# Kernel optimization log

Hardware: AMD Instinct MI355X
Metric: run time of the kernel (lower is better)

The kernel has to match this reference:

```python
import jax, jax.numpy as jnp
import numpy as np

B, S, D = 4, 1024, 768
H = 12
DK = D // H            # 64
NUM_EMB = 10
MAX_DIST = 100000.0 * 2 ** 0.5
POS_SCALE = 100000.0   # tile positions live in [0, 100000]


def setup_inputs() -> dict:
    key = jax.random.key(0)
    ks = jax.random.split(key, 12)
    query = jax.random.normal(ks[0], (B, S, D), dtype=jnp.float32)
    key_t = jax.random.normal(ks[1], (B, S, D), dtype=jnp.float32)
    value = jax.random.normal(ks[2], (B, S, D), dtype=jnp.float32)
    tile_positions = jax.random.uniform(ks[3], (B, S, 2), dtype=jnp.float32) * POS_SCALE
    # Linear weights, torch layout [out, in]; xavier_uniform init, zero bias
    lim = float(np.sqrt(6.0 / (D + D)))
    Wq = jax.random.uniform(ks[4], (D, D), minval=-lim, maxval=lim, dtype=jnp.float32)
    Wk = jax.random.uniform(ks[5], (D, D), minval=-lim, maxval=lim, dtype=jnp.float32)
    Wv = jax.random.uniform(ks[6], (D, D), minval=-lim, maxval=lim, dtype=jnp.float32)
    bq = jnp.zeros((D,), jnp.float32)
    bk = jnp.zeros((D,), jnp.float32)
    bv = jnp.zeros((D,), jnp.float32)
    emb_k = jax.random.normal(ks[7], (NUM_EMB, DK), dtype=jnp.float32)  # nn.Embedding default N(0,1)
    return {"query": query, "key": key_t, "value": value,
            "tile_positions": tile_positions,
            "Wq": Wq, "bq": bq, "Wk": Wk, "bk": bk, "Wv": Wv, "bv": bv,
            "emb_k": emb_k}


def reference(query, key, value, tile_positions, Wq, bq, Wk, bk, Wv, bv, emb_k):
    b, s, _ = query.shape
    # projections -> [B, H, S, DK]
    q = (query @ Wq.T + bq).reshape(b, s, H, DK).transpose(0, 2, 1, 3)
    k = (key   @ Wk.T + bk).reshape(b, s, H, DK).transpose(0, 2, 1, 3)
    v = (value @ Wv.T + bv).reshape(b, s, H, DK).transpose(0, 2, 1, 3)
    # pairwise distances, normalized, discretized to embedding indices
    pos = jax.lax.stop_gradient(tile_positions)
    diff = pos[:, :, None, :] - pos[:, None, :, :]          # [B,S,S,2]
    dist = jnp.sqrt(jnp.sum(diff * diff, axis=-1)) / MAX_DIST  # [B,S,S]
    idx = jnp.clip(jnp.round(dist * (NUM_EMB - 1)), 0, NUM_EMB - 1).astype(jnp.int32)
    rk = emb_k[idx]                                          # [B,S,S,DK]
    # logits: QK^T plus distance-aware key bias
    attn_logits = jnp.einsum('bhqd,bhkd->bhqk', q, k)
    attn_logits = attn_logits + jnp.einsum('bhqd,bqkd->bhqk', q, rk)
    attn_logits = attn_logits / (DK ** 0.5)
    attention = jax.nn.softmax(attn_logits, axis=-1)
    out = jnp.einsum('bhqk,bhkd->bhqd', attention, v)       # [B,H,S,DK]
    out = out.transpose(0, 2, 1, 3).reshape(b, s, -1)       # [B,S,D]
    return out
```

## Files before the change

kernel.cpp:

```cpp
#include <hip/hip_runtime.h>
#include <hip/hip_bf16.h>

#define Bsz 4
#define Ssz 1024
#define Dsz 768
#define Hn 12
#define DKsz 64
#define NUMEMB 10

#define IDX_OFF 64
#define K_OFF   4194368
#define V_OFF   10485824
#define WBF_OFF 16777280
#define XBF_OFF 20316224
#define WS_TIER_B 20316224ULL
#define WS_TIER_A 39190592ULL

#define NXz 3145728
#define NWz 589824

#define IPAD 80

typedef __attribute__((ext_vector_type(8))) short short8;
typedef __attribute__((ext_vector_type(8))) float float8;
typedef __attribute__((ext_vector_type(4))) float f32x4;
typedef __attribute__((ext_vector_type(4))) unsigned int u32x4;

__device__ __forceinline__ float bfbits2f(short u) {
    union { unsigned int i; float f; } v;
    v.i = ((unsigned int)(unsigned short)u) << 16;
    return v.f;
}
__device__ __forceinline__ unsigned short f2bf_bits(float f) {
    __hip_bfloat16 h = __float2bfloat16(f);
    return *reinterpret_cast<unsigned short*>(&h);
}

template<int CTRL>
__device__ __forceinline__ float dppf(float x) {
    int xi = __float_as_int(x);
    int r = __builtin_amdgcn_update_dpp(xi, xi, CTRL, 0xF, 0xF, true);
    return __int_as_float(r);
}
__device__ __forceinline__ float red_max16(float v) {
    v = fmaxf(v, dppf<0xB1>(v));
    v = fmaxf(v, dppf<0x4E>(v));
    v = fmaxf(v, dppf<0x124>(v));
    v = fmaxf(v, dppf<0x128>(v));
    return v;
}
__device__ __forceinline__ float red_sum16(float v) {
    v += dppf<0xB1>(v);
    v += dppf<0x4E>(v);
    v += dppf<0x124>(v);
    v += dppf<0x128>(v);
    return v;
}

template<bool BF16>
__device__ __forceinline__ float loadf(const void* base, size_t idx) {
    if constexpr (BF16) return __bfloat162float(((const __hip_bfloat16*)base)[idx]);
    else return ((const float*)base)[idx];
}
template<bool BF16>
__device__ __forceinline__ short8 load8bf(const void* base, size_t idx) {
    if constexpr (BF16) {
        return *(const short8*)((const short*)base + idx);
    } else {
        float8 f = *(const float8*)((const float*)base + idx);
        short8 r;
#pragma unroll
        for (int i = 0; i < 8; i++) r[i] = (short)f2bf_bits(f[i]);
        return r;
    }
}
template<bool BF16>
__device__ __forceinline__ float8 load8f(const void* base, size_t idx) {
    if constexpr (BF16) {
        short8 s = *(const short8*)((const short*)base + idx);
        float8 f;
#pragma unroll
        for (int i = 0; i < 8; i++) f[i] = bfbits2f(s[i]);
        return f;
    } else {
        return *(const float8*)((const float*)base + idx);
    }
}

__global__ __launch_bounds__(64) void detect_kernel(
    const unsigned int* __restrict__ q, const unsigned int* __restrict__ p,
    const unsigned int* __restrict__ w, const unsigned int* __restrict__ e,
    int* __restrict__ flags)
{
    const int which = blockIdx.x;
    const unsigned int* ptr = (which == 0) ? q : ((which == 1) ? p : ((which == 2) ? w : e));
    const int n = (which == 3) ? 320 : ((which == 1) ? 4096 : 1024);
    int cnt = 0;
    for (int i = threadIdx.x; i < n; i += 64) {
        const unsigned int ex = (ptr[i] >> 7) & 0xFF;
        cnt += (ex >= 110 && ex <= 145) ? 1 : 0;
    }
#pragma unroll
    for (int off = 1; off < 64; off <<= 1) cnt += __shfl_xor(cnt, off, 64);
    if (threadIdx.x == 0) flags[which] = (2 * cnt > n) ? 1 : 0;
}

__global__ __launch_bounds__(256) void conv_kernel(
    const void* __restrict__ X0, const void* __restrict__ X1, const void* __restrict__ X2,
    const void* __restrict__ W0, const void* __restrict__ W1, const void* __restrict__ W2,
    const int* __restrict__ flags, short* __restrict__ Xbf, short* __restrict__ Wbf,
    int doX)
{
    const long t = (long)blockIdx.x * 256 + threadIdx.x;
    const bool xb = flags[0] != 0, wb = flags[2] != 0;
    if (doX) {
        const long i8 = t * 8;
        if (i8 < (long)3 * NXz) {
            const int z = (int)(i8 / NXz);
            const long off = i8 - (long)z * NXz;
            const void* X = (z == 0) ? X0 : ((z == 1) ? X1 : X2);
            short8 v = xb ? load8bf<true>(X, off) : load8bf<false>(X, off);
            *(short8*)(Xbf + i8) = v;
        } else {
            const long j = i8 - (long)3 * NXz;
            const int z = (int)(j / NWz);
            const long off = j - (long)z * NWz;
            const void* W = (z == 0) ? W0 : ((z == 1) ? W1 : W2);
            short8 v = wb ? load8bf<true>(W, off) : load8bf<false>(W, off);
            *(short8*)(Wbf + j) = v;
        }
    } else {
        const long j = t * 8;
        const int z = (int)(j / NWz);
        const long off = j - (long)z * NWz;
        const void* W = (z == 0) ? W0 : ((z == 1) ? W1 : W2);
        short8 v = wb ? load8bf<true>(W, off) : load8bf<false>(W, off);
        *(short8*)(Wbf + j) = v;
    }
}

template<bool PB>
__device__ __forceinline__ void idx_body(
    const void* pos, unsigned char* __restrict__ idxb)
{
    const int kt = blockIdx.x, qt = blockIdx.y, b = blockIdx.z;
    const int t = threadIdx.x;
    const int r = t >> 2, cc = t & 3;
    const int q = qt * 64 + r;
    const float qx = loadf<PB>(pos, ((size_t)b * Ssz + q) * 2);
    const float qy = loadf<PB>(pos, ((size_t)b * Ssz + q) * 2 + 1);
    const float MAXD = 141421.35623730951f;
    const int k0 = kt * 64 + cc * 16;
    unsigned int w[4];
#pragma unroll
    for (int g = 0; g < 4; g++) {
        unsigned int acc = 0;
#pragma unroll
        for (int u = 0; u < 4; u++) {
            const int k = k0 + g * 4 + u;
            const float kx = loadf<PB>(pos, ((size_t)b * Ssz + k) * 2);
            const float ky = loadf<PB>(pos, ((size_t)b * Ssz + k) * 2 + 1);
            const float dx = __fsub_rn(qx, kx);
            const float dy = __fsub_rn(qy, ky);
            const float ss = __fadd_rn(__fmul_rn(dx, dx), __fmul_rn(dy, dy));
            const float dist = __fdiv_rn(sqrtf(ss), MAXD);
            const float d9 = __fmul_rn(dist, 9.0f);
            int idx = (int)rintf(d9);
            idx = idx < 0 ? 0 : (idx > NUMEMB - 1 ? NUMEMB - 1 : idx);
            acc |= ((unsigned int)idx) << (8 * u);
        }
        w[g] = acc;
    }
    u32x4 v; v[0] = w[0]; v[1] = w[1]; v[2] = w[2]; v[3] = w[3];
    *(u32x4*)(idxb + ((size_t)(b * Ssz + q)) * Ssz + k0) = v;
}

__global__ __launch_bounds__(256) void idx_kernel(
    const void* pos, const int* __restrict__ flags, unsigned char* __restrict__ idxb)
{
    if (flags[1] != 0) idx_body<true >(pos, idxb);
    else               idx_body<false>(pos, idxb);
}

template<bool XB, bool WB>
__device__ __forceinline__ void proj_body(
    const void* X, const void* W, const void* bias, bool biasbf, void* Y, bool ybf,
    int bx, int by, short* As, short* Bs)
{
    const int tid  = threadIdx.x;
    const int wave = tid >> 6;
    const int lane = tid & 63;
    const int l15  = lane & 15;
    const int quad = lane >> 4;
    const int wm = wave & 1;
    const int wn = wave >> 1;
    const int m0 = bx * 64;
    const int n0 = by * 128;

    f32x4 acc[2][4];
#pragma unroll
    for (int i = 0; i < 2; i++)
#pragma unroll
        for (int j = 0; j < 4; j++) acc[i][j] = (f32x4)0.0f;

    const int r0 = tid >> 3;
    const int cc = tid & 7;

    short8 pa0 = load8bf<XB>(X, (size_t)(m0 + r0)      * Dsz + cc * 8);
    short8 pa1 = load8bf<XB>(X, (size_t)(m0 + 32 + r0) * Dsz + cc * 8);
    short8 pb0 = load8bf<WB>(W, (size_t)(n0 + r0)      * Dsz + cc * 8);
    short8 pb1 = load8bf<WB>(W, (size_t)(n0 + 32 + r0) * Dsz + cc * 8);
    short8 pb2 = load8bf<WB>(W, (size_t)(n0 + 64 + r0) * Dsz + cc * 8);
    short8 pb3 = load8bf<WB>(W, (size_t)(n0 + 96 + r0) * Dsz + cc * 8);

    for (int kk = 0; kk < Dsz; kk += 64) {
        __syncthreads();
        *(short8*)&As[(r0)      * 72 + cc * 8] = pa0;
        *(short8*)&As[(32 + r0) * 72 + cc * 8] = pa1;
        *(short8*)&Bs[(r0)      * 72 + cc * 8] = pb0;
        *(short8*)&Bs[(32 + r0) * 72 + cc * 8] = pb1;
        *(short8*)&Bs[(64 + r0) * 72 + cc * 8] = pb2;
        *(short8*)&Bs[(96 + r0) * 72 + cc * 8] = pb3;
        __syncthreads();

        if (kk + 64 < Dsz) {
            const int k2 = kk + 64 + cc * 8;
            pa0 = load8bf<XB>(X, (size_t)(m0 + r0)      * Dsz + k2);
            pa1 = load8bf<XB>(X, (size_t)(m0 + 32 + r0) * Dsz + k2);
            pb0 = load8bf<WB>(W, (size_t)(n0 + r0)      * Dsz + k2);
            pb1 = load8bf<WB>(W, (size_t)(n0 + 32 + r0) * Dsz + k2);
            pb2 = load8bf<WB>(W, (size_t)(n0 + 64 + r0) * Dsz + k2);
            pb3 = load8bf<WB>(W, (size_t)(n0 + 96 + r0) * Dsz + k2);
        }

#pragma unroll
        for (int st = 0; st < 2; st++) {
            short8 af[2], bf[4];
#pragma unroll
            for (int i = 0; i < 2; i++)
                af[i] = *(const short8*)&As[(wm * 32 + i * 16 + l15) * 72 + st * 32 + quad * 8];
#pragma unroll
            for (int j = 0; j < 4; j++)
                bf[j] = *(const short8*)&Bs[(wn * 64 + j * 16 + l15) * 72 + st * 32 + quad * 8];
#pragma unroll
            for (int i = 0; i < 2; i++)
#pragma unroll
                for (int j = 0; j < 4; j++)
                    acc[i][j] = __builtin_amdgcn_mfma_f32_16x16x32_bf16(af[i], bf[j], acc[i][j], 0, 0, 0);
        }
    }

#pragma unroll
    for (int j = 0; j < 4; j++) {
        const int n = n0 + wn * 64 + j * 16 + l15;
        const float bv_ = biasbf ? loadf<true>(bias, n) : loadf<false>(bias, n);
#pragma unroll
        for (int i = 0; i < 2; i++) {
#pragma unroll
            for (int r = 0; r < 4; r++) {
                const int m = m0 + wm * 32 + i * 16 + quad * 4 + r;
                const float val = acc[i][j][r] + bv_;
                if (ybf) ((__hip_bfloat16*)Y)[(size_t)m * Dsz + n] = __float2bfloat16(val);
                else     ((float*)Y)[(size_t)m * Dsz + n] = val;
            }
        }
    }
}

__global__ __launch_bounds__(256) void proj_kernel(
    const void* X0, const void* X1, const void* X2,
    const void* Wq, const void* bq, const void* Wk, const void* bk,
    const void* Wv, const void* bv,
    void* Qw, void* Kw, void* Vw, const int* __restrict__ flags,
    int fx, int fw)
{
    __shared__ __align__(16) short As[64 * 72];
    __shared__ __align__(16) short Bs[128 * 72];
    const int z = blockIdx.z;
    const void* X = (z == 0) ? X0 : ((z == 1) ? X1 : X2);
    const void* W = (z == 0) ? Wq : ((z == 1) ? Wk : Wv);
    const void* B = (z == 0) ? bq : ((z == 1) ? bk : bv);
    void* Y = (z == 0) ? Qw : ((z == 1) ? Kw : Vw);
    const bool xb = fx || flags[0] != 0;
    const bool wb = fw || flags[2] != 0;
    const bool biasbf = flags[2] != 0;
    const bool ybf = (flags[0] != 0) || (z != 0);
    if (xb) { if (wb) proj_body<true , true >(X, W, B, biasbf, Y, ybf, blockIdx.x, blockIdx.y, As, Bs);
              else    proj_body<true , false>(X, W, B, biasbf, Y, ybf, blockIdx.x, blockIdx.y, As, Bs); }
    else    { if (wb) proj_body<false, true >(X, W, B, biasbf, Y, ybf, blockIdx.x, blockIdx.y, As, Bs);
              else    proj_body<false, false>(X, W, B, biasbf, Y, ybf, blockIdx.x, blockIdx.y, As, Bs); }
}

template<bool QB, bool EB>
__device__ __forceinline__ void attn_body(
    const void* Qw, const short* __restrict__ Ks, const short* __restrict__ Vs,
    const unsigned char* __restrict__ idxb, const void* __restrict__ emb, void* out,
    unsigned short* Klds, unsigned short* Vtlds, unsigned short* Plds,
    float* qe, unsigned char* Ilds)
{
    const int qt = blockIdx.x, h = blockIdx.y, b = blockIdx.z;
    const int tid  = threadIdx.x;
    const int wave = tid >> 6;
    const int lane = tid & 63;
    const int l15  = lane & 15;
    const int quad = lane >> 4;

    for (int p = tid; p < 64 * NUMEMB; p += 256) {
        const int row = p / NUMEMB, e = p - row * NUMEMB;
        const size_t qoff = ((size_t)b * Ssz + qt * 64 + row) * Dsz + h * DKsz;
        float s = 0.f;
#pragma unroll
        for (int c = 0; c < 8; c++) {
            short8 qv = load8bf<QB>(Qw, qoff + c * 8);
            float8 ef = load8f<EB>(emb, (size_t)e * DKsz + c * 8);
#pragma unroll
            for (int i = 0; i < 8; i++) s += bfbits2f(qv[i]) * ef[i];
        }
        qe[p] = s;
    }

    short8 qfrag[2];
    {
        const size_t qbase = ((size_t)b * Ssz + qt * 64 + wave * 16 + l15) * Dsz + h * DKsz;
        qfrag[0] = load8bf<QB>(Qw, qbase + quad * 8);
        qfrag[1] = load8bf<QB>(Qw, qbase + 32 + quad * 8);
    }

    float m_run[4], l_run[4];
    f32x4 oacc[4];
#pragma unroll
    for (int r = 0; r < 4; r++) { m_run[r] = -1e30f; l_run[r] = 0.f; }
#pragma unroll
    for (int j = 0; j < 4; j++) oacc[j] = (f32x4)0.0f;

    const int srow = tid >> 3, schk = tid & 7;
    const int vp   = tid >> 3;
    const int irow = tid >> 2, ichk = tid & 3;

    short8 pk0, pk1, pv0, pv1;
    u32x4 pidx;
    {
        pk0 = *(const short8*)(Ks + ((size_t)b * Ssz + srow)       * Dsz + h * DKsz + schk * 8);
        pk1 = *(const short8*)(Ks + ((size_t)b * Ssz + 32 + srow)  * Dsz + h * DKsz + schk * 8);
        pv0 = *(const short8*)(Vs + ((size_t)b * Ssz + 2 * vp)     * Dsz + h * DKsz + schk * 8);
        pv1 = *(const short8*)(Vs + ((size_t)b * Ssz + 2 * vp + 1) * Dsz + h * DKsz + schk * 8);
        pidx = *(const u32x4*)(idxb + ((size_t)(b * Ssz + irow)) * Ssz + qt * 64 + ichk * 16);
    }

    for (int it = 0; it < 16; it++) {
        __syncthreads();
        *(short8*)&Klds[(srow)      * 72 + schk * 8] = pk0;
        *(short8*)&Klds[(32 + srow) * 72 + schk * 8] = pk1;
        {
            const int ssw = (2 * vp) ^ (schk << 3);
#pragma unroll
            for (int i = 0; i < 8; i++) {
                const unsigned int dw = (unsigned int)(unsigned short)pv0[i]
                                      | ((unsigned int)(unsigned short)pv1[i] << 16);
                *(unsigned int*)&Vtlds[(schk * 8 + i) * 72 + ssw] = dw;
            }
        }
        *(u32x4*)&Ilds[irow * IPAD + ichk * 16] = pidx;
        __syncthreads();

        if (it + 1 < 16) {
            const size_t kb = ((size_t)b * Ssz + (it + 1) * 64) * Dsz + h * DKsz;
            pk0 = *(const short8*)(Ks + kb + (size_t)srow * Dsz + schk * 8);
            pk1 = *(const short8*)(Ks + kb + (size_t)(32 + srow) * Dsz + schk * 8);
            pv0 = *(const short8*)(Vs + kb + (size_t)(2 * vp) * Dsz + schk * 8);
            pv1 = *(const short8*)(Vs + kb + (size_t)(2 * vp + 1) * Dsz + schk * 8);
            pidx = *(const u32x4*)(idxb + ((size_t)(b * Ssz + (it + 1) * 64 + irow)) * Ssz + qt * 64 + ichk * 16);
        }

        f32x4 sf[4];
#pragma unroll
        for (int j = 0; j < 4; j++) sf[j] = (f32x4)0.0f;
#pragma unroll
        for (int st = 0; st < 2; st++) {
#pragma unroll
            for (int j = 0; j < 4; j++) {
                short8 kb2 = *(const short8*)&Klds[(j * 16 + l15) * 72 + st * 32 + quad * 8];
                sf[j] = __builtin_amdgcn_mfma_f32_16x16x32_bf16(qfrag[st], kb2, sf[j], 0, 0, 0);
            }
        }

        float sv[4][4];
#pragma unroll
        for (int j = 0; j < 4; j++) {
            const unsigned int iw = *(const unsigned int*)&Ilds[(j * 16 + l15) * IPAD + wave * 16 + quad * 4];
#pragma unroll
            for (int r = 0; r < 4; r++) {
                const int m = wave * 16 + quad * 4 + r;
                const int idx = (iw >> (8 * r)) & 0xFF;
                sv[r][j] = (sf[j][r] + qe[m * NUMEMB + idx]) * 0.125f;
            }
        }

        float alpha[4];
#pragma unroll
        for (int r = 0; r < 4; r++) {
            float vmax = fmaxf(fmaxf(sv[r][0], sv[r][1]), fmaxf(sv[r][2], sv[r][3]));
            vmax = red_max16(vmax);
            const float mnew = fmaxf(m_run[r], vmax);
            alpha[r] = __expf(m_run[r] - mnew);
            m_run[r] = mnew;
            float psum = 0.f;
#pragma unroll
            for (int j = 0; j < 4; j++) {
                const float p = __expf(sv[r][j] - mnew);
                sv[r][j] = p;
                psum += p;
            }
            psum = red_sum16(psum);
            l_run[r] = l_run[r] * alpha[r] + psum;
        }
#pragma unroll
        for (int j = 0; j < 4; j++) {
            f32x4 o = oacc[j];
#pragma unroll
            for (int r = 0; r < 4; r++) o[r] *= alpha[r];
            oacc[j] = o;
        }

#pragma unroll
        for (int r = 0; r < 4; r++) {
            const int m = wave * 16 + quad * 4 + r;
#pragma unroll
            for (int j = 0; j < 4; j++) {
                const int csw = (j * 16 + l15) ^ (quad << 4);
                Plds[m * 72 + csw] = f2bf_bits(sv[r][j]);
            }
        }

#pragma unroll
        for (int st = 0; st < 2; st++) {
            const int prow = wave * 16 + l15;
            const int pcsw = (st * 32 + quad * 8) ^ ((l15 >> 2) << 4);
            short8 pf = *(const short8*)&Plds[prow * 72 + pcsw];
#pragma unroll
            for (int j = 0; j < 4; j++) {
                const int d = j * 16 + l15;
                const int vsw = (st * 32 + quad * 8) ^ (((d >> 3) & 7) << 3);
                short8 vb = *(const short8*)&Vtlds[d * 72 + vsw];
                oacc[j] = __builtin_amdgcn_mfma_f32_16x16x32_bf16(pf, vb, oacc[j], 0, 0, 0);
            }
        }
    }

    __syncthreads();

#pragma unroll
    for (int r = 0; r < 4; r++) {
        const float inv = 1.0f / l_run[r];
        const int m = qt * 64 + wave * 16 + quad * 4 + r;
#pragma unroll
        for (int j = 0; j < 4; j++) {
            const int n = h * DKsz + j * 16 + l15;
            const float val = oacc[j][r] * inv;
            const size_t oidx = ((size_t)b * Ssz + m) * Dsz + n;
            if constexpr (QB) ((__hip_bfloat16*)out)[oidx] = __float2bfloat16(val);
            else              ((float*)out)[oidx] = val;
        }
    }
}

__global__ __launch_bounds__(256) void attn_kernel(
    const void* Qw, const short* __restrict__ Ks, const short* __restrict__ Vs,
    const unsigned char* __restrict__ idxb, const void* __restrict__ emb, void* out,
    const int* __restrict__ flags)
{
    __shared__ __align__(16) unsigned short Klds[64 * 72];
    __shared__ __align__(16) unsigned short Vtlds[64 * 72];
    __shared__ __align__(16) unsigned short Plds[64 * 72];
    __shared__ __align__(16) float qe[64 * NUMEMB];
    __shared__ __align__(16) unsigned char Ilds[64 * IPAD];

    const bool qb = flags[0] != 0, eb = flags[3] != 0;
    if (qb) { if (eb) attn_body<true , true >(Qw, Ks, Vs, idxb, emb, out, Klds, Vtlds, Plds, qe, Ilds);
              else    attn_body<true , false>(Qw, Ks, Vs, idxb, emb, out, Klds, Vtlds, Plds, qe, Ilds); }
    else    { if (eb) attn_body<false, true >(Qw, Ks, Vs, idxb, emb, out, Klds, Vtlds, Plds, qe, Ilds);
              else    attn_body<false, false>(Qw, Ks, Vs, idxb, emb, out, Klds, Vtlds, Plds, qe, Ilds); }
}

extern "C" void kernel_launch(void* const* d_in, const int* in_sizes, int n_in,
                              void* d_out, int out_size, void* d_ws, size_t ws_size,
                              hipStream_t stream) {
    const void* query = d_in[0];
    const void* key   = d_in[1];
    const void* value = d_in[2];
    const void* tpos  = d_in[3];
    const void* Wq    = d_in[4];
    const void* bq    = d_in[5];
    const void* Wk    = d_in[6];
    const void* bk    = d_in[7];
    const void* Wv    = d_in[8];
    const void* bv    = d_in[9];
    const void* emb   = d_in[10];

    int*           flags = (int*)d_ws;
    unsigned char* idxb  = (unsigned char*)d_ws + IDX_OFF;
    void*          Kw    = (char*)d_ws + K_OFF;
    void*          Vw    = (char*)d_ws + V_OFF;
    short*         Wbf   = (short*)((char*)d_ws + WBF_OFF);
    short*         Xbf   = (short*)((char*)d_ws + XBF_OFF);
    void*          Qw    = d_out;

    const bool tierA = ws_size >= WS_TIER_A;
    const bool tierB = !tierA && ws_size >= WS_TIER_B;

    detect_kernel<<<4, 64, 0, stream>>>(
        (const unsigned int*)query, (const unsigned int*)tpos,
        (const unsigned int*)Wq, (const unsigned int*)emb, flags);

    if (tierA)
        conv_kernel<<<5472, 256, 0, stream>>>(query, key, value, Wq, Wk, Wv, flags, Xbf, Wbf, 1);
    else if (tierB)
        conv_kernel<<<864, 256, 0, stream>>>(query, key, value, Wq, Wk, Wv, flags, Xbf, Wbf, 0);

    idx_kernel<<<dim3(16, 16, Bsz), 256, 0, stream>>>(tpos, flags, idxb);

    if (tierA)
        proj_kernel<<<dim3(64, 6, 3), 256, 0, stream>>>(
            Xbf, Xbf + NXz, Xbf + 2 * NXz,
            Wbf, bq, Wbf + NWz, bk, Wbf + 2 * NWz, bv,
            Qw, Kw, Vw, flags, 1, 1);
    else if (tierB)
        proj_kernel<<<dim3(64, 6, 3), 256, 0, stream>>>(
            query, key, value,
            Wbf, bq, Wbf + NWz, bk, Wbf + 2 * NWz, bv,
            Qw, Kw, Vw, flags, 0, 1);
    else
        proj_kernel<<<dim3(64, 6, 3), 256, 0, stream>>>(
            query, key, value, Wq, bq, Wk, bk, Wv, bv,
            Qw, Kw, Vw, flags, 0, 0);

    attn_kernel<<<dim3(16, Hn, Bsz), 256, 0, stream>>>(
        Qw, (const short*)Kw, (const short*)Vw, idxb, emb, d_out, flags);
}
```

Baseline: 220.2 us.

## Emit head-major K and transposed V, double-buffer attention tiles, use exp2 softmax

The projection epilogue now writes K in [B,H,S,DK] layout and V pre-transposed as [B,H,DK,S], so the attention kernel no longer transposes V when storing it to shared memory. The attention loop double-buffers K/V tiles in shared memory with one barrier per iteration. Distance indices are read straight from global memory into registers, replacing the shared-memory staging. The softmax folds log2(e) into the scale so it can use exp2f, and MFMA sections are bracketed with s_setprio. The cost is twice the K/V shared memory, which may reduce occupancy, plus strided 4-byte index loads.

```diff
diff --git a/kernel.cpp b/kernel.cpp
--- a/kernel.cpp
+++ b/kernel.cpp
@@ -19,12 +19,11 @@
 #define NXz 3145728
 #define NWz 589824
 
-#define IPAD 80
-
 typedef __attribute__((ext_vector_type(8))) short short8;
 typedef __attribute__((ext_vector_type(8))) float float8;
 typedef __attribute__((ext_vector_type(4))) float f32x4;
 typedef __attribute__((ext_vector_type(4))) unsigned int u32x4;
+typedef __attribute__((ext_vector_type(4))) short s16x4;
 
 __device__ __forceinline__ float bfbits2f(short u) {
     union { unsigned int i; float f; } v;
@@ -185,7 +184,7 @@
 template<bool XB, bool WB>
 __device__ __forceinline__ void proj_body(
     const void* X, const void* W, const void* bias, bool biasbf, void* Y, bool ybf,
-    int bx, int by, short* As, short* Bs)
+    int zmode, int bx, int by, short* As, short* Bs)
 {
     const int tid  = threadIdx.x;
     const int wave = tid >> 6;
@@ -254,14 +253,30 @@
     for (int j = 0; j < 4; j++) {
         const int n = n0 + wn * 64 + j * 16 + l15;
         const float bv_ = biasbf ? loadf<true>(bias, n) : loadf<false>(bias, n);
+        const int hh = n >> 6, dk = n & 63;
 #pragma unroll
         for (int i = 0; i < 2; i++) {
-#pragma unroll
-            for (int r = 0; r < 4; r++) {
-                const int m = m0 + wm * 32 + i * 16 + quad * 4 + r;
-                const float val = acc[i][j][r] + bv_;
-                if (ybf) ((__hip_bfloat16*)Y)[(size_t)m * Dsz + n] = __float2bfloat16(val);
-                else     ((float*)Y)[(size_t)m * Dsz + n] = val;
+            const int ms = m0 + wm * 32 + i * 16 + quad * 4;
+            const int bb = ms >> 10;
+            const int s0 = ms & 1023;
+            if (zmode == 2) {
+                s16x4 pkv;
+#pragma unroll
+                for (int r = 0; r < 4; r++) pkv[r] = (short)f2bf_bits(acc[i][j][r] + bv_);
+                *(s16x4*)((short*)Y + (((size_t)bb * Hn + hh) * DKsz + dk) * Ssz + s0) = pkv;
+            } else if (zmode == 1) {
+#pragma unroll
+                for (int r = 0; r < 4; r++)
+                    ((__hip_bfloat16*)Y)[(((size_t)bb * Hn + hh) * Ssz + (s0 + r)) * DKsz + dk] =
+                        __float2bfloat16(acc[i][j][r] + bv_);
+            } else {
+#pragma unroll
+                for (int r = 0; r < 4; r++) {
+                    const float val = acc[i][j][r] + bv_;
+                    const size_t oi = (size_t)(ms + r) * Dsz + n;
+                    if (ybf) ((__hip_bfloat16*)Y)[oi] = __float2bfloat16(val);
+                    else     ((float*)Y)[oi] = val;
+                }
             }
         }
     }
@@ -285,18 +300,17 @@
     const bool wb = fw || flags[2] != 0;
     const bool biasbf = flags[2] != 0;
     const bool ybf = (flags[0] != 0) || (z != 0);
-    if (xb) { if (wb) proj_body<true , true >(X, W, B, biasbf, Y, ybf, blockIdx.x, blockIdx.y, As, Bs);
-              else    proj_body<true , false>(X, W, B, biasbf, Y, ybf, blockIdx.x, blockIdx.y, As, Bs); }
-    else    { if (wb) proj_body<false, true >(X, W, B, biasbf, Y, ybf, blockIdx.x, blockIdx.y, As, Bs);
-              else    proj_body<false, false>(X, W, B, biasbf, Y, ybf, blockIdx.x, blockIdx.y, As, Bs); }
+    if (xb) { if (wb) proj_body<true , true >(X, W, B, biasbf, Y, ybf, z, blockIdx.x, blockIdx.y, As, Bs);
+              else    proj_body<true , false>(X, W, B, biasbf, Y, ybf, z, blockIdx.x, blockIdx.y, As, Bs); }
+    else    { if (wb) proj_body<false, true >(X, W, B, biasbf, Y, ybf, z, blockIdx.x, blockIdx.y, As, Bs);
+              else    proj_body<false, false>(X, W, B, biasbf, Y, ybf, z, blockIdx.x, blockIdx.y, As, Bs); }
 }
 
 template<bool QB, bool EB>
 __device__ __forceinline__ void attn_body(
     const void* Qw, const short* __restrict__ Ks, const short* __restrict__ Vs,
     const unsigned char* __restrict__ idxb, const void* __restrict__ emb, void* out,
-    unsigned short* Klds, unsigned short* Vtlds, unsigned short* Plds,
-    float* qe, unsigned char* Ilds)
+    unsigned short* Klds, unsigned short* Vtlds, unsigned short* Plds, float* qe)
 {
     const int qt = blockIdx.x, h = blockIdx.y, b = blockIdx.z;
     const int tid  = threadIdx.x;
@@ -333,66 +347,71 @@
 #pragma unroll
     for (int j = 0; j < 4; j++) oacc[j] = (f32x4)0.0f;
 
-    const int srow = tid >> 3, schk = tid & 7;
-    const int vp   = tid >> 3;
-    const int irow = tid >> 2, ichk = tid & 3;
-
-    short8 pk0, pk1, pv0, pv1;
-    u32x4 pidx;
-    {
-        pk0 = *(const short8*)(Ks + ((size_t)b * Ssz + srow)       * Dsz + h * DKsz + schk * 8);
-        pk1 = *(const short8*)(Ks + ((size_t)b * Ssz + 32 + srow)  * Dsz + h * DKsz + schk * 8);
-        pv0 = *(const short8*)(Vs + ((size_t)b * Ssz + 2 * vp)     * Dsz + h * DKsz + schk * 8);
-        pv1 = *(const short8*)(Vs + ((size_t)b * Ssz + 2 * vp + 1) * Dsz + h * DKsz + schk * 8);
-        pidx = *(const u32x4*)(idxb + ((size_t)(b * Ssz + irow)) * Ssz + qt * 64 + ichk * 16);
-    }
-
-    for (int it = 0; it < 16; it++) {
-        __syncthreads();
-        *(short8*)&Klds[(srow)      * 72 + schk * 8] = pk0;
-        *(short8*)&Klds[(32 + srow) * 72 + schk * 8] = pk1;
-        {
-            const int ssw = (2 * vp) ^ (schk << 3);
-#pragma unroll
-            for (int i = 0; i < 8; i++) {
-                const unsigned int dw = (unsigned int)(unsigned short)pv0[i]
-                                      | ((unsigned int)(unsigned short)pv1[i] << 16);
-                *(unsigned int*)&Vtlds[(schk * 8 + i) * 72 + ssw] = dw;
-            }
-        }
-        *(u32x4*)&Ilds[irow * IPAD + ichk * 16] = pidx;
-        __syncthreads();
+    const int lds_off = (tid >> 3) * 72 + (tid & 7) * 8;
+    const short* kp = Ks + ((size_t)(b * Hn + h) * Ssz) * DKsz + tid * 8;
+    const short* vp = Vs + ((size_t)(b * Hn + h) * DKsz + (tid >> 3)) * Ssz + (tid & 7) * 8;
+    const unsigned char* ip = idxb + ((size_t)b * Ssz + l15) * Ssz
+                                   + (size_t)qt * 64 + wave * 16 + quad * 4;
+
+    short8 pk0 = *(const short8*)(kp);
+    short8 pk1 = *(const short8*)(kp + 2048);
+    short8 pv0 = *(const short8*)(vp);
+    short8 pv1 = *(const short8*)(vp + 32 * Ssz);
+    unsigned int id0 = *(const unsigned int*)(ip);
+    unsigned int id1 = *(const unsigned int*)(ip + 16 * Ssz);
+    unsigned int id2 = *(const unsigned int*)(ip + 32 * Ssz);
+    unsigned int id3 = *(const unsigned int*)(ip + 48 * Ssz);
+
+    *(short8*)&Klds[lds_off]           = pk0;
+    *(short8*)&Klds[32 * 72 + lds_off] = pk1;
+    *(short8*)&Vtlds[lds_off]           = pv0;
+    *(short8*)&Vtlds[32 * 72 + lds_off] = pv1;
+    __syncthreads();
+
+    const float CSC = 0.18033688011112042f;
+
+    for (int it = 0; it < 16; ++it) {
+        const int cur = (it & 1) ? (64 * 72) : 0;
+        const int nxt = (it & 1) ? 0 : (64 * 72);
+        const unsigned int jd[4] = { id0, id1, id2, id3 };
 
         if (it + 1 < 16) {
-            const size_t kb = ((size_t)b * Ssz + (it + 1) * 64) * Dsz + h * DKsz;
-            pk0 = *(const short8*)(Ks + kb + (size_t)srow * Dsz + schk * 8);
-            pk1 = *(const short8*)(Ks + kb + (size_t)(32 + srow) * Dsz + schk * 8);
-            pv0 = *(const short8*)(Vs + kb + (size_t)(2 * vp) * Dsz + schk * 8);
-            pv1 = *(const short8*)(Vs + kb + (size_t)(2 * vp + 1) * Dsz + schk * 8);
-            pidx = *(const u32x4*)(idxb + ((size_t)(b * Ssz + (it + 1) * 64 + irow)) * Ssz + qt * 64 + ichk * 16);
+            kp += 4096;
+            vp += 64;
+            ip += (size_t)64 * Ssz;
+            pk0 = *(const short8*)(kp);
+            pk1 = *(const short8*)(kp + 2048);
+            pv0 = *(const short8*)(vp);
+            pv1 = *(const short8*)(vp + 32 * Ssz);
+            id0 = *(const unsigned int*)(ip);
+            id1 = *(const unsigned int*)(ip + 16 * Ssz);
+            id2 = *(const unsigned int*)(ip + 32 * Ssz);
+            id3 = *(const unsigned int*)(ip + 48 * Ssz);
         }
 
         f32x4 sf[4];
 #pragma unroll
         for (int j = 0; j < 4; j++) sf[j] = (f32x4)0.0f;
+        __builtin_amdgcn_s_setprio(1);
 #pragma unroll
         for (int st = 0; st < 2; st++) {
 #pragma unroll
             for (int j = 0; j < 4; j++) {
-                short8 kb2 = *(const short8*)&Klds[(j * 16 + l15) * 72 + st * 32 + quad * 8];
+                short8 kb2 = *(const short8*)&Klds[cur + (j * 16 + l15) * 72 + st * 32 + quad * 8];
                 sf[j] = __builtin_amdgcn_mfma_f32_16x16x32_bf16(qfrag[st], kb2, sf[j], 0, 0, 0);
             }
         }
+        __builtin_amdgcn_s_setprio(0);
 
         float sv[4][4];
 #pragma unroll
         for (int j = 0; j < 4; j++) {
-            const unsigned int iw = *(const unsigned int*)&Ilds[(j * 16 + l15) * IPAD + wave * 16 + quad * 4];
+            const unsigned int iw = jd[j];
 #pragma unroll
             for (int r = 0; r < 4; r++) {
                 const int m = wave * 16 + quad * 4 + r;
                 const int idx = (iw >> (8 * r)) & 0xFF;
-                sv[r][j] = (sf[j][r] + qe[m * NUMEMB + idx]) * 0.125f;
+                sv[r][j] = (sf[j][r] + qe[m * NUMEMB + idx]) * CSC;
             }
         }
 
@@ -402,12 +421,12 @@
             float vmax = fmaxf(fmaxf(sv[r][0], sv[r][1]), fmaxf(sv[r][2], sv[r][3]));
             vmax = red_max16(vmax);
             const float mnew = fmaxf(m_run[r], vmax);
-            alpha[r] = __expf(m_run[r] - mnew);
+            alpha[r] = exp2f(m_run[r] - mnew);
             m_run[r] = mnew;
             float psum = 0.f;
 #pragma unroll
             for (int j = 0; j < 4; j++) {
-                const float p = __expf(sv[r][j] - mnew);
+                const float p = exp2f(sv[r][j] - mnew);
                 sv[r][j] = p;
                 psum += p;
             }
@@ -432,6 +451,7 @@
             }
         }
 
+        __builtin_amdgcn_s_setprio(1);
 #pragma unroll
         for (int st = 0; st < 2; st++) {
             const int prow = wave * 16 + l15;
@@ -439,15 +459,20 @@
             short8 pf = *(const short8*)&Plds[prow * 72 + pcsw];
 #pragma unroll
             for (int j = 0; j < 4; j++) {
-                const int d = j * 16 + l15;
-                const int vsw = (st * 32 + quad * 8) ^ (((d >> 3) & 7) << 3);
-                short8 vb = *(const short8*)&Vtlds[d * 72 + vsw];
+                short8 vb = *(const short8*)&Vtlds[cur + (j * 16 + l15) * 72 + st * 32 + quad * 8];
                 oacc[j] = __builtin_amdgcn_mfma_f32_16x16x32_bf16(pf, vb, oacc[j], 0, 0, 0);
             }
         }
-    }
-
-    __syncthreads();
+        __builtin_amdgcn_s_setprio(0);
+
+        if (it + 1 < 16) {
+            *(short8*)&Klds[nxt + lds_off]           = pk0;
+            *(short8*)&Klds[nxt + 32 * 72 + lds_off] = pk1;
+            *(short8*)&Vtlds[nxt + lds_off]           = pv0;
+            *(short8*)&Vtlds[nxt + 32 * 72 + lds_off] = pv1;
+        }
+        __syncthreads();
+    }
 
 #pragma unroll
     for (int r = 0; r < 4; r++) {
@@ -469,17 +494,16 @@
     const unsigned char* __restrict__ idxb, const void* __restrict__ emb, void* out,
     const int* __restrict__ flags)
 {
-    __shared__ __align__(16) unsigned short Klds[64 * 72];
-    __shared__ __align__(16) unsigned short Vtlds[64 * 72];
+    __shared__ __align__(16) unsigned short Klds[2 * 64 * 72];
+    __shared__ __align__(16) unsigned short Vtlds[2 * 64 * 72];
     __shared__ __align__(16) unsigned short Plds[64 * 72];
     __shared__ __align__(16) float qe[64 * NUMEMB];
-    __shared__ __align__(16) unsigned char Ilds[64 * IPAD];
 
     const bool qb = flags[0] != 0, eb = flags[3] != 0;
-    if (qb) { if (eb) attn_body<true , true >(Qw, Ks, Vs, idxb, emb, out, Klds, Vtlds, Plds, qe, Ilds);
-              else    attn_body<true , false>(Qw, Ks, Vs, idxb, emb, out, Klds, Vtlds, Plds, qe, Ilds); }
-    else    { if (eb) attn_body<false, true >(Qw, Ks, Vs, idxb, emb, out, Klds, Vtlds, Plds, qe, Ilds);
-              else    attn_body<false, false>(Qw, Ks, Vs, idxb, emb, out, Klds, Vtlds, Plds, qe, Ilds); }
+    if (qb) { if (eb) attn_body<true , true >(Qw, Ks, Vs, idxb, emb, out, Klds, Vtlds, Plds, qe);
+              else    attn_body<true , false>(Qw, Ks, Vs, idxb, emb, out, Klds, Vtlds, Plds, qe); }
+    else    { if (eb) attn_body<false, true >(Qw, Ks, Vs, idxb, emb, out, Klds, Vtlds, Plds, qe);
+              else    attn_body<false, false>(Qw, Ks, Vs, idxb, emb, out, Klds, Vtlds, Plds, qe); }
 }
 
 extern "C" void kernel_launch(void* const* d_in, const int* in_sizes, int n_in,
```

After: 220.2 us. Within noise of the previous version (-0.0%).
